# Optimization experiments

Measured on AMD Instinct MI355X. Metric: run time of the kernel, lower is better.

Reference implementation:

```python
import jax, jax.numpy as jnp
import numpy as np

K, D = 512, 2048
B, T = 32, 512

def setup_inputs() -> dict:
    key = jax.random.key(0)
    k1, k2, k3, k4 = jax.random.split(key, 4)
    z_e_x = jax.random.normal(k1, (B, D, T), dtype=jnp.float32)
    # embedding.weight.data.uniform_(-1/K, 1/K)
    codebook = jax.random.uniform(k2, (K, D), dtype=jnp.float32, minval=-1.0 / K, maxval=1.0 / K)
    # Conv1d(2048, 1, 1): weight (1, 2048, 1) -> stored as (D,), bias (1,)
    bound = 1.0 / np.sqrt(D)
    conv_w = jax.random.uniform(k3, (D,), dtype=jnp.float32, minval=-bound, maxval=bound)
    conv_b = jax.random.uniform(k4, (1,), dtype=jnp.float32, minval=-bound, maxval=bound)
    return {"z_e_x": z_e_x, "codebook": codebook, "conv_w": conv_w, "conv_b": conv_b}

def _vq_indices(flat, codebook):
    # flat: (N, D), codebook: (K, D); squared L2 distances via expansion
    dists = (
        jnp.sum(flat * flat, axis=1, keepdims=True)
        - 2.0 * flat @ codebook.T
        + jnp.sum(codebook * codebook, axis=1)[None, :]
    )  # (N, K)
    return jnp.argmin(dists, axis=1)  # (N,)

def _conv1x1(x, conv_w, conv_b):
    # Conv1d(D, 1, kernel=1) on (B, D, T) -> (B, 1, T)
    return jnp.einsum('bdt,d->bt', x, conv_w)[:, None, :] + conv_b[None, :, None]

def reference(z_e_x, codebook, conv_w, conv_b):
    # Faithful to VQEmbedding.straight_through (superset of forward's vq)
    z = jnp.transpose(z_e_x, (0, 2, 1))            # (B, T, D)
    flat = z.reshape(-1, D)                         # (N, D)
    indices = _vq_indices(flat, codebook)           # (N,) == forward()'s latents (flattened)
    quant = codebook[indices].reshape(z.shape)      # (B, T, D)
    # vq_st: straight-through estimator (codebook detached, grad copies to z_e_x)
    z_q_ = z + jax.lax.stop_gradient(quant - z)
    z_q_x = jnp.transpose(z_q_, (0, 2, 1))          # (B, D, T)
    z_q_x_onehot = _conv1x1(z_q_x, conv_w, conv_b)  # (B, 1, T)
    # index_select on non-detached embedding weight -> grads flow to codebook here
    z_q_x_bar = jnp.transpose(quant, (0, 2, 1))     # (B, D, T)
    z_q_x_bar_onehot = _conv1x1(z_q_x_bar, conv_w, conv_b)
    return (z_q_x, z_q_x_onehot, z_q_x_bar, z_q_x_bar_onehot)
```

## Files before the change

kernel.cpp:

```cpp
#include <hip/hip_runtime.h>
#include <cstdint>

#define Dd 2048
#define Tt 512
#define Bb 32
#define Kc 512
#define Nn 16384

typedef _Float16 half8 __attribute__((ext_vector_type(8)));
typedef float f32x4 __attribute__((ext_vector_type(4)));

__device__ __forceinline__ float sqf(float v) { return v * v; }

__device__ __forceinline__ unsigned int fenc(float f) {
  unsigned int u = __float_as_uint(f);
  return (u & 0x80000000u) ? ~u : (u | 0x80000000u);
}

__device__ __forceinline__ unsigned long long ullmin(unsigned long long a,
                                                     unsigned long long b) {
  return b < a ? b : a;
}

__device__ __forceinline__ void gload_lds16(const _Float16* g, _Float16* l) {
  __builtin_amdgcn_global_load_lds(
      (const __attribute__((address_space(1))) void*)g,
      (__attribute__((address_space(3))) void*)l, 16, 0, 0);
}


__global__ __launch_bounds__(256) void k_splitz(const float* __restrict__ z,
                                                _Float16* __restrict__ zh,
                                                _Float16* __restrict__ zl,
                                                float* __restrict__ Bc) {
  __shared__ float sbuf[64 * 130];
  __shared__ float Ps[4 * 64];
  const int tid = threadIdx.x;
  const int t0  = blockIdx.x * 64;
  const int b   = blockIdx.y;
  const int cg  = blockIdx.z;
  const int tt  = tid & 63;
  const int w   = tid >> 6;

  for (int ci = 0; ci < 4; ++ci) {
    const int c = cg * 4 + ci;
    const float* zp = z + (size_t)b * Dd * Tt + (size_t)(c * 128) * Tt + t0;
    __syncthreads();
    #pragma unroll
    for (int i = 0; i < 32; ++i) {
      const int d = i * 4 + w;
      sbuf[tt * 130 + d] = zp[(size_t)d * Tt + tt];
    }
    __syncthreads();
    {
      const float* row = &sbuf[tt * 130];
      const int j = 2 * w;
      float r0 = sqf(row[j]);
      float r1 = sqf(row[j + 1]);
      #pragma unroll
      for (int s = 1; s < 16; ++s) {
        r0 += sqf(row[j + 8 * s]);
        r1 += sqf(row[j + 1 + 8 * s]);
      }
      Ps[w * 64 + tt] = r0 + r1;
    }
    {
      const int chunk = tid & 15;
      const int rr    = tid >> 4;
      #pragma unroll
      for (int p = 0; p < 4; ++p) {
        const int t = p * 16 + rr;
        const float* src = &sbuf[t * 130 + chunk * 8];
        __align__(16) _Float16 hbuf[8], lbuf[8];
        #pragma unroll
        for (int jj = 0; jj < 8; ++jj) {
          float v = src[jj];
          _Float16 h = (_Float16)v;
          hbuf[jj] = h;
          lbuf[jj] = (_Float16)((v - (float)h) * 4096.f);
        }
        const size_t off = (size_t)(b * Tt + t0 + t) * Dd + c * 128 + chunk * 8;
        *(float4*)(zh + off) = *(float4*)hbuf;
        *(float4*)(zl + off) = *(float4*)lbuf;
      }
    }
    __syncthreads();
    if (tid < 64) {
      const float B = (Ps[tid] + Ps[64 + tid]) + (Ps[128 + tid] + Ps[192 + tid]);
      Bc[c * Nn + b * Tt + t0 + tid] = B;
    }
  }
}

__global__ __launch_bounds__(256) void k_prep2(const float* __restrict__ cb,
                                               const float* __restrict__ w,
                                               float* __restrict__ cnorm,
                                               float* __restrict__ qd,
                                               _Float16* __restrict__ chp,
                                               _Float16* __restrict__ clp) {
  __shared__ float Bs[16 * 16];
  __shared__ float Qs[16 * 16];
  const int tid = threadIdx.x;
  const int kl  = tid >> 4;
  const int blk = tid & 15;
  const int k = blockIdx.x * 16 + kl;
  const float* row = cb + (size_t)k * Dd + blk * 128;
  const float* wp  = w + blk * 128;
  _Float16* ch_o = chp + (size_t)k * Dd + blk * 128;
  _Float16* cl_o = clp + (size_t)k * Dd + blk * 128;
  __align__(16) _Float16 hbuf[8], lbuf[8];
  float r[8];
  float q = 0.f;
  for (int s = 0; s < 16; ++s) {
    #pragma unroll
    for (int j = 0; j < 8; ++j) {
      int p = s * 8 + j;
      float v = row[p];
      float sq = v * v;
      if (s == 0) r[j] = sq; else r[j] += sq;
      q = fmaf(v, wp[p], q);
      _Float16 h = (_Float16)v;
      hbuf[j] = h;
      lbuf[j] = (_Float16)((v - (float)h) * 4096.f);
    }
    *(float4*)(ch_o + s * 8) = *(float4*)hbuf;
    *(float4*)(cl_o + s * 8) = *(float4*)lbuf;
  }
  float B = ((r[0] + r[1]) + (r[2] + r[3])) + ((r[4] + r[5]) + (r[6] + r[7]));
  Bs[kl * 16 + blk] = B;
  Qs[kl * 16 + blk] = q;
  __syncthreads();
  if (blk == 0) {
    const float* bb = &Bs[kl * 16];
    float d0 = (bb[0] + bb[1]) + (bb[2] + bb[3]);
    float d1 = (bb[4] + bb[5]) + (bb[6] + bb[7]);
    float d2 = (bb[8] + bb[9]) + (bb[10] + bb[11]);
    float d3 = (bb[12] + bb[13]) + (bb[14] + bb[15]);
    cnorm[k] = (d0 + d1) + (d2 + d3);
    const float* qq = &Qs[kl * 16];
    float s = 0.f;
    #pragma unroll
    for (int i = 0; i < 16; ++i) s += qq[i];
    qd[k] = s;
  }
}

__global__ __launch_bounds__(256) void k_prep_nb(const float* __restrict__ cb,
                                                 const float* __restrict__ w,
                                                 float* __restrict__ cnorm,
                                                 float* __restrict__ qd) {
  __shared__ float Bs[16 * 16];
  __shared__ float Qs[16 * 16];
  const int tid = threadIdx.x;
  const int kl  = tid >> 4;
  const int blk = tid & 15;
  const int k = blockIdx.x * 16 + kl;
  const float* row = cb + (size_t)k * Dd + blk * 128;
  const float* wp  = w + blk * 128;
  float r[8];
  float q = 0.f;
  for (int s = 0; s < 16; ++s) {
    #pragma unroll
    for (int j = 0; j < 8; ++j) {
      int p = s * 8 + j;
      float v = row[p];
      float sq = v * v;
      if (s == 0) r[j] = sq; else r[j] += sq;
      q = fmaf(v, wp[p], q);
    }
  }
  float B = ((r[0] + r[1]) + (r[2] + r[3])) + ((r[4] + r[5]) + (r[6] + r[7]));
  Bs[kl * 16 + blk] = B;
  Qs[kl * 16 + blk] = q;
  __syncthreads();
  if (blk == 0) {
    const float* bb = &Bs[kl * 16];
    float d0 = (bb[0] + bb[1]) + (bb[2] + bb[3]);
    float d1 = (bb[4] + bb[5]) + (bb[6] + bb[7]);
    float d2 = (bb[8] + bb[9]) + (bb[10] + bb[11]);
    float d3 = (bb[12] + bb[13]) + (bb[14] + bb[15]);
    cnorm[k] = (d0 + d1) + (d2 + d3);
    const float* qq = &Qs[kl * 16];
    float s = 0.f;
    #pragma unroll
    for (int i = 0; i < 16; ++i) s += qq[i];
    qd[k] = s;
  }
}

__global__ __launch_bounds__(256, 3) void k_gemm_mfma(
    const _Float16* __restrict__ zh, const _Float16* __restrict__ zl,
    const _Float16* __restrict__ ch, const _Float16* __restrict__ cl,
    const float* __restrict__ Bc, const float* __restrict__ cnorm,
    unsigned long long* __restrict__ keys) {
  const int n0 = blockIdx.x * 128;
  const int k0 = blockIdx.y * 128;

  __shared__ __align__(16) _Float16 smem[4 * 128 * 32];
  __shared__ unsigned long long keybuf[128][2];
  __shared__ float xn_s[128];

  const int tid = threadIdx.x;

  if (tid < 128) {
    const int n = n0 + tid;
    float bb[16];
    #pragma unroll
    for (int c = 0; c < 16; ++c) bb[c] = Bc[c * Nn + n];
    float d0 = (bb[0] + bb[1]) + (bb[2] + bb[3]);
    float d1 = (bb[4] + bb[5]) + (bb[6] + bb[7]);
    float d2 = (bb[8] + bb[9]) + (bb[10] + bb[11]);
    float d3 = (bb[12] + bb[13]) + (bb[14] + bb[15]);
    xn_s[tid] = (d0 + d1) + (d2 + d3);
  }

  const int lane = tid & 63;
  const int wid  = tid >> 6;
  const int wr   = wid >> 1, wc = wid & 1;
  const int lrow = lane & 15, lq = lane >> 4;

  f32x4 acc_h[4][4], acc_x[4][4];
  #pragma unroll
  for (int i = 0; i < 4; ++i)
    #pragma unroll
    for (int j = 0; j < 4; ++j) {
      acc_h[i][j] = (f32x4)0.f;
      acc_x[i][j] = (f32x4)0.f;
    }

  const int srow = tid >> 2;
  const int scol = (tid & 3) * 8;
  const _Float16* gsrc0 = zh + (size_t)(n0 + srow) * Dd + scol;
  const _Float16* gsrc1 = zl + (size_t)(n0 + srow) * Dd + scol;
  const _Float16* gsrc2 = ch + (size_t)(k0 + srow) * Dd + scol;
  const _Float16* gsrc3 = cl + (size_t)(k0 + srow) * Dd + scol;
  _Float16* ldst = smem + tid * 8;

  const _Float16* Ah = smem;
  const _Float16* Al = smem + 4096;
  const _Float16* Bh = smem + 8192;
  const _Float16* Bl = smem + 12288;
  const size_t half_skip = (size_t)64 * Dd;

  for (int dt = 0; dt < Dd / 32; ++dt) {
    const int doff = dt * 32;
    __syncthreads();
    gload_lds16(gsrc0 + doff,             ldst);
    gload_lds16(gsrc0 + half_skip + doff, ldst + 2048);
    gload_lds16(gsrc1 + doff,             ldst + 4096);
    gload_lds16(gsrc1 + half_skip + doff, ldst + 6144);
    gload_lds16(gsrc2 + doff,             ldst + 8192);
    gload_lds16(gsrc2 + half_skip + doff, ldst + 10240);
    gload_lds16(gsrc3 + doff,             ldst + 12288);
    gload_lds16(gsrc3 + half_skip + doff, ldst + 14336);
    __syncthreads();

    half8 ah[4], al[4];
    #pragma unroll
    for (int i = 0; i < 4; ++i) {
      int row = wr * 64 + i * 16 + lrow;
      ah[i] = *(const half8*)&Ah[row * 32 + lq * 8];
      al[i] = *(const half8*)&Al[row * 32 + lq * 8];
    }
    #pragma unroll
    for (int j = 0; j < 4; ++j) {
      int row = wc * 64 + j * 16 + lrow;
      half8 bh = *(const half8*)&Bh[row * 32 + lq * 8];
      half8 bl = *(const half8*)&Bl[row * 32 + lq * 8];
      #pragma unroll
      for (int i = 0; i < 4; ++i) {
        acc_h[i][j] = __builtin_amdgcn_mfma_f32_16x16x32_f16(ah[i], bh, acc_h[i][j], 0, 0, 0);
        acc_x[i][j] = __builtin_amdgcn_mfma_f32_16x16x32_f16(ah[i], bl, acc_x[i][j], 0, 0, 0);
        acc_x[i][j] = __builtin_amdgcn_mfma_f32_16x16x32_f16(al[i], bh, acc_x[i][j], 0, 0, 0);
      }
    }
  }

  float cn[4];
  #pragma unroll
  for (int j = 0; j < 4; ++j) cn[j] = cnorm[k0 + wc * 64 + j * 16 + lrow];

  #pragma unroll
  for (int i = 0; i < 4; ++i) {
    #pragma unroll
    for (int reg = 0; reg < 4; ++reg) {
      const int rowl = wr * 64 + i * 16 + lq * 4 + reg;
      const float xn = xn_s[rowl];
      unsigned long long best = ~0ull;
      #pragma unroll
      for (int j = 0; j < 4; ++j) {
        float dot = acc_h[i][j][reg] + acc_x[i][j][reg] * 0x1p-12f;
        float d = fmaf(-2.f, dot, xn) + cn[j];
        unsigned int code = (unsigned int)(k0 + wc * 64 + j * 16 + lrow);
        unsigned long long key = ((unsigned long long)fenc(d) << 32) | code;
        best = ullmin(best, key);
      }
      #pragma unroll
      for (int m = 1; m < 16; m <<= 1)
        best = ullmin(best, (unsigned long long)__shfl_xor((unsigned long long)best, m, 64));
      if (lrow == 0) keybuf[rowl][wc] = best;
    }
  }
  __syncthreads();
  if (tid < 128) {
    unsigned long long kk = ullmin(keybuf[tid][0], keybuf[tid][1]);
    atomicMin(&keys[n0 + tid], kk);
  }
}

__global__ __launch_bounds__(256) void k_scatter(const float* __restrict__ cb,
                                                 const unsigned long long* __restrict__ keys,
                                                 const float* __restrict__ qd,
                                                 const float* __restrict__ bconv,
                                                 float* __restrict__ out0,
                                                 float* __restrict__ out1,
                                                 float* __restrict__ out2,
                                                 float* __restrict__ out3) {
  const int d0 = blockIdx.x * 16;
  const int b  = blockIdx.y;
  __shared__ float cb_s[512 * 17];
  const int tid = threadIdx.x;
  {
    const int kk = tid >> 2;
    const int dq = tid & 3;
    #pragma unroll
    for (int p = 0; p < 8; ++p) {
      int k = p * 64 + kk;
      float4 v = *(const float4*)(cb + (size_t)k * Dd + d0 + dq * 4);
      cb_s[k * 17 + dq * 4 + 0] = v.x;
      cb_s[k * 17 + dq * 4 + 1] = v.y;
      cb_s[k * 17 + dq * 4 + 2] = v.z;
      cb_s[k * 17 + dq * 4 + 3] = v.w;
    }
  }
  const int t4 = (tid & 127) * 4;
  const unsigned long long* kp = keys + b * Tt + t4;
  int4 idx4;
  idx4.x = (int)(kp[0] & 0xFFFFFFFFull);
  idx4.y = (int)(kp[1] & 0xFFFFFFFFull);
  idx4.z = (int)(kp[2] & 0xFFFFFFFFull);
  idx4.w = (int)(kp[3] & 0xFFFFFFFFull);
  if (blockIdx.x == 0 && tid < 128) {
    const float bc0 = bconv[0];
    float4 o1;
    o1.x = qd[idx4.x] + bc0;
    o1.y = qd[idx4.y] + bc0;
    o1.z = qd[idx4.z] + bc0;
    o1.w = qd[idx4.w] + bc0;
    *(float4*)(out1 + b * Tt + t4) = o1;
    *(float4*)(out3 + b * Tt + t4) = o1;
  }
  __syncthreads();
  const int dhalf = tid >> 7;
  #pragma unroll
  for (int p = 0; p < 8; ++p) {
    int dd = p * 2 + dhalf;
    float4 o;
    o.x = cb_s[idx4.x * 17 + dd];
    o.y = cb_s[idx4.y * 17 + dd];
    o.z = cb_s[idx4.z * 17 + dd];
    o.w = cb_s[idx4.w * 17 + dd];
    size_t off = (size_t)b * Dd * Tt + (size_t)(d0 + dd) * Tt + t4;
    *(float4*)(out0 + off) = o;
    *(float4*)(out2 + off) = o;
  }
}


__global__ __launch_bounds__(256) void k_xnorm(const float* __restrict__ z,
                                               float* __restrict__ xnorm) {
  const int t0 = blockIdx.x * 64;
  const int b  = blockIdx.y;
  __shared__ float sbuf[128 * 64];
  __shared__ float Ps[256];
  __shared__ float Bs2[64 * 16];
  const int tid = threadIdx.x;
  const int tt = tid & 63;
  const int j2 = tid >> 6;
  const float* zb = z + (size_t)b * Dd * Tt + t0;
  for (int c = 0; c < 16; ++c) {
    __syncthreads();
    #pragma unroll
    for (int it = 0; it < 32; ++it) {
      int d = j2 + it * 4;
      sbuf[d * 64 + tt] = zb[(size_t)(c * 128 + d) * Tt + tt];
    }
    __syncthreads();
    float r0, r1;
    {
      const int j = 2 * j2;
      r0 = sqf(sbuf[j * 64 + tt]);
      #pragma unroll
      for (int s = 1; s < 16; ++s) r0 += sqf(sbuf[(j + 8 * s) * 64 + tt]);
      r1 = sqf(sbuf[(j + 1) * 64 + tt]);
      #pragma unroll
      for (int s = 1; s < 16; ++s) r1 += sqf(sbuf[(j + 1 + 8 * s) * 64 + tt]);
    }
    Ps[j2 * 64 + tt] = r0 + r1;
    __syncthreads();
    if (tid < 64) {
      float B = (Ps[tid] + Ps[64 + tid]) + (Ps[128 + tid] + Ps[192 + tid]);
      Bs2[tid * 16 + c] = B;
    }
  }
  __syncthreads();
  if (tid < 64) {
    const float* bb = &Bs2[tid * 16];
    float d0 = (bb[0] + bb[1]) + (bb[2] + bb[3]);
    float d1 = (bb[4] + bb[5]) + (bb[6] + bb[7]);
    float d2 = (bb[8] + bb[9]) + (bb[10] + bb[11]);
    float d3 = (bb[12] + bb[13]) + (bb[14] + bb[15]);
    xnorm[b * Tt + t0 + tid] = (d0 + d1) + (d2 + d3);
  }
}

__global__ __launch_bounds__(256, 2) void k_gemm(const float* __restrict__ z,
                                                 const float* __restrict__ cb,
                                                 const float* __restrict__ cnorm,
                                                 const float* __restrict__ xnorm,
                                                 unsigned long long* __restrict__ keys) {
  const int n0 = blockIdx.x * 128;
  const int k0 = blockIdx.y * 128;
  const int b  = n0 >> 9;
  const int t0 = n0 & 511;
  const float* zbase = z + (size_t)b * Dd * Tt + t0;

  __shared__ __align__(16) float As[32 * 132];
  __shared__ __align__(16) float Cs[32 * 132];
  __shared__ float red_v[16 * 128];
  __shared__ int   red_i[16 * 128];

  const int tid = threadIdx.x;
  const int t4a = (tid & 31) * 4;
  const int dla = tid >> 5;
  const int kc  = tid >> 3;
  const int dq  = tid & 7;
  const int r0  = (tid & 15) * 8;
  const int c0  = (tid >> 4) * 8;

  float4 pa[4], pc[4];
  {
    #pragma unroll
    for (int p = 0; p < 4; ++p)
      pa[p] = *(const float4*)(zbase + (size_t)(dla + p * 8) * Tt + t4a);
    const float* cp = cb + (size_t)(k0 + kc) * Dd + dq * 4;
    #pragma unroll
    for (int p = 0; p < 4; ++p)
      pc[p] = *(const float4*)(cp + (size_t)p * 32 * Dd);
  }

  float acc[8][8];
  #pragma unroll
  for (int i = 0; i < 8; ++i)
    #pragma unroll
    for (int j = 0; j < 8; ++j) acc[i][j] = 0.f;

  for (int dt = 0; dt < Dd / 32; ++dt) {
    __syncthreads();
    #pragma unroll
    for (int p = 0; p < 4; ++p)
      *(float4*)&As[(dla + p * 8) * 132 + t4a] = pa[p];
    #pragma unroll
    for (int p = 0; p < 4; ++p) {
      Cs[(dq * 4 + 0) * 132 + kc + p * 32] = pc[p].x;
      Cs[(dq * 4 + 1) * 132 + kc + p * 32] = pc[p].y;
      Cs[(dq * 4 + 2) * 132 + kc + p * 32] = pc[p].z;
      Cs[(dq * 4 + 3) * 132 + kc + p * 32] = pc[p].w;
    }
    __syncthreads();
    if (dt + 1 < Dd / 32) {
      const float* zp = zbase + (size_t)(dt + 1) * 32 * Tt;
      #pragma unroll
      for (int p = 0; p < 4; ++p)
        pa[p] = *(const float4*)(zp + (size_t)(dla + p * 8) * Tt + t4a);
      const float* cp = cb + (size_t)(k0 + kc) * Dd + (dt + 1) * 32 + dq * 4;
      #pragma unroll
      for (int p = 0; p < 4; ++p)
        pc[p] = *(const float4*)(cp + (size_t)p * 32 * Dd);
    }
    #pragma unroll 8
    for (int dl = 0; dl < 32; ++dl) {
      float4 a0 = *(const float4*)&As[dl * 132 + r0];
      float4 a1 = *(const float4*)&As[dl * 132 + r0 + 4];
      float4 b0 = *(const float4*)&Cs[dl * 132 + c0];
      float4 b1 = *(const float4*)&Cs[dl * 132 + c0 + 4];
      float av[8] = {a0.x, a0.y, a0.z, a0.w, a1.x, a1.y, a1.z, a1.w};
      float bv[8] = {b0.x, b0.y, b0.z, b0.w, b1.x, b1.y, b1.z, b1.w};
      #pragma unroll
      for (int i = 0; i < 8; ++i)
        #pragma unroll
        for (int j = 0; j < 8; ++j)
          acc[i][j] = fmaf(av[i], bv[j], acc[i][j]);
    }
  }

  float cn[8];
  #pragma unroll
  for (int j = 0; j < 8; ++j) cn[j] = cnorm[k0 + c0 + j];
  float xnv[8];
  #pragma unroll
  for (int i = 0; i < 8; ++i) xnv[i] = xnorm[n0 + r0 + i];

  const int c16 = tid >> 4;
  #pragma unroll
  for (int i = 0; i < 8; ++i) {
    float bv = fmaf(-2.f, acc[i][0], xnv[i]) + cn[0];
    int bi = 0;
    #pragma unroll
    for (int j = 1; j < 8; ++j) {
      float d = fmaf(-2.f, acc[i][j], xnv[i]) + cn[j];
      if (d < bv) { bv = d; bi = j; }
    }
    red_v[c16 * 128 + r0 + i] = bv;
    red_i[c16 * 128 + r0 + i] = k0 + c0 + bi;
  }
  __syncthreads();
  if (tid < 128) {
    float bv = red_v[tid];
    int bi = red_i[tid];
    #pragma unroll
    for (int j = 1; j < 16; ++j) {
      float v = red_v[j * 128 + tid];
      if (v < bv) { bv = v; bi = red_i[j * 128 + tid]; }
    }
    unsigned long long key = ((unsigned long long)fenc(bv) << 32) | (unsigned int)bi;
    atomicMin(&keys[n0 + tid], key);
  }
}


extern "C" void kernel_launch(void* const* d_in, const int* in_sizes, int n_in,
                              void* d_out, int out_size, void* d_ws, size_t ws_size,
                              hipStream_t stream) {
  const float* z  = (const float*)d_in[0];
  const float* cb = (const float*)d_in[1];
  const float* w  = (const float*)d_in[2];
  const float* bc = (const float*)d_in[3];

  float* out0 = (float*)d_out;
  float* out1 = out0 + (size_t)Bb * Dd * Tt;
  float* out2 = out1 + (size_t)Bb * Tt;
  float* out3 = out2 + (size_t)Bb * Dd * Tt;

  char* ws = (char*)d_ws;
  unsigned long long* keys = (unsigned long long*)ws;
  float* cnorm = (float*)(ws + 131072);
  float* qd    = (float*)(ws + 133120);
  float* xnorm = (float*)(ws + 200704);
  float* Bc    = (float*)(ws + 266240);
  _Float16* chp = (_Float16*)(ws + 1314816);
  _Float16* clp = (_Float16*)(ws + 3411968);
  _Float16* zh  = (_Float16*)(ws + 5509120);
  _Float16* zl  = (_Float16*)(ws + 72617984);
  const size_t need = 139726848;

  hipMemsetAsync(keys, 0xFF, (size_t)Nn * 8, stream);

  if (ws_size >= need) {
    k_splitz<<<dim3(Tt / 64, Bb, 4), dim3(256), 0, stream>>>(z, zh, zl, Bc);
    k_prep2<<<dim3(Kc / 16), dim3(256), 0, stream>>>(cb, w, cnorm, qd, chp, clp);
    k_gemm_mfma<<<dim3(Nn / 128, Kc / 128), dim3(256), 0, stream>>>(
        zh, zl, chp, clp, Bc, cnorm, keys);
  } else {
    k_xnorm<<<dim3(Tt / 64, Bb), dim3(256), 0, stream>>>(z, xnorm);
    k_prep_nb<<<dim3(Kc / 16), dim3(256), 0, stream>>>(cb, w, cnorm, qd);
    k_gemm<<<dim3(Nn / 128, Kc / 128), dim3(256), 0, stream>>>(z, cb, cnorm, xnorm, keys);
  }
  k_scatter<<<dim3(Dd / 16, Bb), dim3(256), 0, stream>>>(cb, keys, qd, bc,
                                                         out0, out1, out2, out3);
}
```

Baseline: 600.2 us.

## Double-buffer LDS tiles in the MFMA distance GEMM and swizzle LDS columns

Replaces the single-buffered load/sync/compute loop with a two-stage ping-pong LDS pipeline. The next K-slice's global-to-LDS loads are issued before computing on the current buffer, with explicit vmcnt waits and raw barriers. It also XOR-swizzles LDS column placement to cut bank conflicts on the half8 fragment reads. LDS use doubles, so launch bounds drop from 3 to 2 blocks per CU, trading occupancy for latency hiding.

```diff
diff --git a/kernel.cpp b/kernel.cpp
--- a/kernel.cpp
+++ b/kernel.cpp
@@ -188,7 +188,41 @@
   }
 }
 
-__global__ __launch_bounds__(256, 3) void k_gemm_mfma(
+#define GSTAGE(dtv, bufp) do {                                       \
+    const int doff_ = (dtv) * 32;                                    \
+    gload_lds16(gsrc0 + doff_,             (bufp) + st_off);         \
+    gload_lds16(gsrc0 + half_skip + doff_, (bufp) + st_off + 2048);  \
+    gload_lds16(gsrc1 + doff_,             (bufp) + 4096 + st_off);  \
+    gload_lds16(gsrc1 + half_skip + doff_, (bufp) + 4096 + st_off + 2048); \
+    gload_lds16(gsrc2 + doff_,             (bufp) + 8192 + st_off);  \
+    gload_lds16(gsrc2 + half_skip + doff_, (bufp) + 8192 + st_off + 2048); \
+    gload_lds16(gsrc3 + doff_,             (bufp) + 12288 + st_off); \
+    gload_lds16(gsrc3 + half_skip + doff_, (bufp) + 12288 + st_off + 2048); \
+  } while (0)
+
+#define GCOMPUTE(bufp) do {                                          \
+    half8 ah_[4], al_[4];                                            \
+    _Pragma("unroll")                                                \
+    for (int i = 0; i < 4; ++i) {                                    \
+      const int row_ = wr * 64 + i * 16 + lrow;                      \
+      ah_[i] = *(const half8*)&(bufp)[row_ * 32 + cq];               \
+      al_[i] = *(const half8*)&(bufp)[4096 + row_ * 32 + cq];        \
+    }                                                                \
+    _Pragma("unroll")                                                \
+    for (int j = 0; j < 4; ++j) {                                    \
+      const int rowb_ = wc * 64 + j * 16 + lrow;                     \
+      half8 bh_ = *(const half8*)&(bufp)[8192 + rowb_ * 32 + cq];    \
+      half8 bl_ = *(const half8*)&(bufp)[12288 + rowb_ * 32 + cq];   \
+      _Pragma("unroll")                                              \
+      for (int i = 0; i < 4; ++i) {                                  \
+        acc_h[i][j] = __builtin_amdgcn_mfma_f32_16x16x32_f16(ah_[i], bh_, acc_h[i][j], 0, 0, 0); \
+        acc_x[i][j] = __builtin_amdgcn_mfma_f32_16x16x32_f16(ah_[i], bl_, acc_x[i][j], 0, 0, 0); \
+        acc_x[i][j] = __builtin_amdgcn_mfma_f32_16x16x32_f16(al_[i], bh_, acc_x[i][j], 0, 0, 0); \
+      }                                                              \
+    }                                                                \
+  } while (0)
+
+__global__ __launch_bounds__(256, 2) void k_gemm_mfma(
     const _Float16* __restrict__ zh, const _Float16* __restrict__ zl,
     const _Float16* __restrict__ ch, const _Float16* __restrict__ cl,
     const float* __restrict__ Bc, const float* __restrict__ cnorm,
@@ -196,9 +230,11 @@
   const int n0 = blockIdx.x * 128;
   const int k0 = blockIdx.y * 128;
 
-  __shared__ __align__(16) _Float16 smem[4 * 128 * 32];
+  __shared__ __align__(16) _Float16 smem[2 * 4 * 128 * 32];
   __shared__ unsigned long long keybuf[128][2];
   __shared__ float xn_s[128];
+  _Float16* buf0 = smem;
+  _Float16* buf1 = smem + 16384;
 
   const int tid = threadIdx.x;
 
@@ -218,6 +254,7 @@
   const int wid  = tid >> 6;
   const int wr   = wid >> 1, wc = wid & 1;
   const int lrow = lane & 15, lq = lane >> 4;
+  const int cq = (lq ^ ((lrow >> 1) & 3)) * 8;
 
   f32x4 acc_h[4][4], acc_x[4][4];
   #pragma unroll
@@ -229,51 +266,35 @@
     }
 
   const int srow = tid >> 2;
-  const int scol = (tid & 3) * 8;
+  const int ssw  = (srow >> 1) & 3;
+  const int scol = ((tid & 3) ^ ssw) * 8;
+  const int st_off = tid * 8;
   const _Float16* gsrc0 = zh + (size_t)(n0 + srow) * Dd + scol;
   const _Float16* gsrc1 = zl + (size_t)(n0 + srow) * Dd + scol;
   const _Float16* gsrc2 = ch + (size_t)(k0 + srow) * Dd + scol;
   const _Float16* gsrc3 = cl + (size_t)(k0 + srow) * Dd + scol;
-  _Float16* ldst = smem + tid * 8;
-
-  const _Float16* Ah = smem;
-  const _Float16* Al = smem + 4096;
-  const _Float16* Bh = smem + 8192;
-  const _Float16* Bl = smem + 12288;
   const size_t half_skip = (size_t)64 * Dd;
 
-  for (int dt = 0; dt < Dd / 32; ++dt) {
-    const int doff = dt * 32;
-    __syncthreads();
-    gload_lds16(gsrc0 + doff,             ldst);
-    gload_lds16(gsrc0 + half_skip + doff, ldst + 2048);
-    gload_lds16(gsrc1 + doff,             ldst + 4096);
-    gload_lds16(gsrc1 + half_skip + doff, ldst + 6144);
-    gload_lds16(gsrc2 + doff,             ldst + 8192);
-    gload_lds16(gsrc2 + half_skip + doff, ldst + 10240);
-    gload_lds16(gsrc3 + doff,             ldst + 12288);
-    gload_lds16(gsrc3 + half_skip + doff, ldst + 14336);
-    __syncthreads();
-
-    half8 ah[4], al[4];
-    #pragma unroll
-    for (int i = 0; i < 4; ++i) {
-      int row = wr * 64 + i * 16 + lrow;
-      ah[i] = *(const half8*)&Ah[row * 32 + lq * 8];
-      al[i] = *(const half8*)&Al[row * 32 + lq * 8];
-    }
-    #pragma unroll
-    for (int j = 0; j < 4; ++j) {
-      int row = wc * 64 + j * 16 + lrow;
-      half8 bh = *(const half8*)&Bh[row * 32 + lq * 8];
-      half8 bl = *(const half8*)&Bl[row * 32 + lq * 8];
-      #pragma unroll
-      for (int i = 0; i < 4; ++i) {
-        acc_h[i][j] = __builtin_amdgcn_mfma_f32_16x16x32_f16(ah[i], bh, acc_h[i][j], 0, 0, 0);
-        acc_x[i][j] = __builtin_amdgcn_mfma_f32_16x16x32_f16(ah[i], bl, acc_x[i][j], 0, 0, 0);
-        acc_x[i][j] = __builtin_amdgcn_mfma_f32_16x16x32_f16(al[i], bh, acc_x[i][j], 0, 0, 0);
-      }
-    }
+  GSTAGE(0, buf0);
+  #pragma unroll 1
+  for (int dt = 0; dt < 64; dt += 2) {
+    GSTAGE(dt + 1, buf1);
+    asm volatile("s_waitcnt vmcnt(8)" ::: "memory");
+    __builtin_amdgcn_s_barrier();
+    GCOMPUTE(buf0);
+    asm volatile("s_waitcnt lgkmcnt(0)" ::: "memory");
+    __builtin_amdgcn_s_barrier();
+
+    if (dt + 2 < 64) {
+      GSTAGE(dt + 2, buf0);
+      asm volatile("s_waitcnt vmcnt(8)" ::: "memory");
+    } else {
+      asm volatile("s_waitcnt vmcnt(0)" ::: "memory");
+    }
+    __builtin_amdgcn_s_barrier();
+    GCOMPUTE(buf1);
+    asm volatile("s_waitcnt lgkmcnt(0)" ::: "memory");
+    __builtin_amdgcn_s_barrier();
   }
 
   float cn[4];
```

Result: faster. 530.8 us (-11.6%).
